# Kernel tuning notes

Measured on AMD Instinct MI355X. Metric: run time of the kernel, lower is better.

Reference implementation:

```python
import jax, jax.numpy as jnp
import numpy as np
import math

VOCAB, EMBED, RES = 50257, 512, 2048
B, T = 64, 512
LN_EPS = 1e-5


def setup_inputs() -> dict:
    key = jax.random.key(0)
    k_x, k_e, k_r, k_w = jax.random.split(key, 4)
    x = jax.random.randint(k_x, (B, T), 0, VOCAB)
    embed_weight = jax.random.normal(k_e, (VOCAB, EMBED), dtype=jnp.float32)
    R = jax.random.normal(k_r, (RES, RES), dtype=jnp.float32) / math.sqrt(RES) / 0.9
    Win = jax.random.normal(k_w, (EMBED, RES), dtype=jnp.float32) / math.sqrt(EMBED) / 0.9
    gamma = jnp.ones((RES,), dtype=jnp.float32)
    beta = jnp.zeros((RES,), dtype=jnp.float32)
    return {"x": x, "embed_weight": embed_weight, "R": R, "Win": Win,
            "gamma": gamma, "beta": beta}


def reference(x, embed_weight, R, Win, gamma, beta):
    emb = embed_weight[x]                              # [B, T, E]
    inp = jnp.einsum('bte,er->btr', emb, Win)          # [B, T, RES]

    def step(state, u_t):                              # state: [B, RES]
        new_state = jnp.tanh(state @ R + u_t)
        return new_state, None

    state0 = jnp.zeros((x.shape[0], R.shape[0]), dtype=emb.dtype)
    state, _ = jax.lax.scan(step, state0, jnp.swapaxes(inp, 0, 1))  # scan over T

    # LayerNorm over last dim (eps=1e-5, affine)
    mu = jnp.mean(state, axis=-1, keepdims=True)
    var = jnp.mean((state - mu) ** 2, axis=-1, keepdims=True)
    normed = (state - mu) / jnp.sqrt(var + LN_EPS)
    return normed * gamma + beta
```

## Files before the change

kernel.cpp:

```cpp
#include <hip/hip_runtime.h>

#define BB 64
#define TT 512
#define EE 512
#define RR 2048
#define CPW 32
#define RPG 16
#define NWGS 256
#define FPAD 16
#define SLOTB (BB * RR * 4)
#define GRPB  (RPG * RR * 4)
#define SPIN_CAP (1 << 20)

typedef _Float16 f16;
typedef f16 f16x8 __attribute__((ext_vector_type(8)));
typedef float f32x4 __attribute__((ext_vector_type(4)));

__device__ __forceinline__ void gload16(const void* g, void* l) {
  __builtin_amdgcn_global_load_lds(
      (const __attribute__((address_space(1))) void*)g,
      (__attribute__((address_space(3))) void*)l, 16, 0, 0);
}

__device__ __forceinline__ float fast_tanh(float v) {
  float e = __expf(2.0f * v);
  return 1.0f - 2.0f / (e + 1.0f);
}

__device__ __forceinline__ void storeS(f16* p, f16 h) {
  union { f16 h; unsigned short s; } u;
  u.h = h;
  __hip_atomic_store((unsigned short*)p, u.s, __ATOMIC_RELAXED, __HIP_MEMORY_SCOPE_AGENT);
}

__device__ __forceinline__ unsigned flag_ld(const unsigned* p) {
  return __hip_atomic_load(p, __ATOMIC_RELAXED, __HIP_MEMORY_SCOPE_AGENT);
}
__device__ __forceinline__ void flag_st(unsigned* p, unsigned v) {
  __hip_atomic_store(p, v, __ATOMIC_RELAXED, __HIP_MEMORY_SCOPE_AGENT);
}

__device__ __forceinline__ void issue8(f16x8* dst, unsigned voff, const f16* sbase) {
#pragma unroll
  for (int i = 0; i < 8; ++i)
    asm volatile("global_load_dwordx4 %0, %1, %2 offset:%c3"
                 : "=v"(dst[i]) : "v"(voff), "s"(sbase), "i"(64 * i) : "memory");
}

__device__ __forceinline__ float bypass_ldf(unsigned voff, const float* base) {
  float v;
  asm volatile("global_load_dword %0, %1, %2 sc0 sc1"
               : "=v"(v) : "v"(voff), "s"(base) : "memory");
  return v;
}

template <int N>
__device__ __forceinline__ void wait_vm() {
  asm volatile("s_waitcnt vmcnt(%c0)" :: "i"(N) : "memory");
  __builtin_amdgcn_sched_barrier(0);
}


__global__ void prep_emb(const int* __restrict__ x, const float* __restrict__ ew,
                         f16* __restrict__ emb) {
  const int row = blockIdx.x;
  const int tok = x[row];
  const float4* src = (const float4*)(ew + (size_t)tok * EE);
  f16* dst = emb + (size_t)row * EE;
  const int i = threadIdx.x;
  float4 v = src[i];
  union { f16 h[4]; unsigned long long u; } p;
  p.h[0] = (f16)v.x; p.h[1] = (f16)v.y; p.h[2] = (f16)v.z; p.h[3] = (f16)v.w;
  ((unsigned long long*)dst)[i] = p.u;
}

__global__ void prep_winT(const float* __restrict__ Win, f16* __restrict__ WinT) {
  const int i = blockIdx.x * blockDim.x + threadIdx.x;
  if (i < EE * RR) {
    const int k = i / RR, n = i % RR;
    WinT[(size_t)n * EE + k] = (f16)Win[i];
  }
}


__launch_bounds__(256, 1)
__global__ void proj_gemm(const f16* __restrict__ A, const f16* __restrict__ Bt,
                          float* __restrict__ U) {
  __shared__ f16 As[128 * 32];
  __shared__ f16 Bs[128 * 32];
  const int tid = threadIdx.x;
  const int wv = tid >> 6, l = tid & 63;
  const int m0 = blockIdx.x * 128, n0 = blockIdx.y * 128;
  const int wm = wv >> 1, wn = wv & 1;
  const int srow = tid >> 2, sc = tid & 3;
  const int r = l & 15, kb = l >> 4;
  f32x4 acc[4][4] = {};

  for (int k0 = 0; k0 < EE; k0 += 32) {
    __syncthreads();
#pragma unroll
    for (int q = 0; q < 2; ++q) {
      const int row = q * 64 + srow;
      const int cc = sc ^ (row & 3);
      gload16(A + (size_t)(m0 + row) * EE + k0 + cc * 8,
              (char*)As + q * 4096 + wv * 1024);
      gload16(Bt + (size_t)(n0 + row) * EE + k0 + cc * 8,
              (char*)Bs + q * 4096 + wv * 1024);
    }
    __syncthreads();
    f16x8 af[4], bf[4];
#pragma unroll
    for (int mi = 0; mi < 4; ++mi) {
      const int row = wm * 64 + mi * 16 + r;
      af[mi] = *(const f16x8*)&As[row * 32 + ((kb ^ (row & 3)) * 8)];
    }
#pragma unroll
    for (int ni = 0; ni < 4; ++ni) {
      const int row = wn * 64 + ni * 16 + r;
      bf[ni] = *(const f16x8*)&Bs[row * 32 + ((kb ^ (row & 3)) * 8)];
    }
#pragma unroll
    for (int mi = 0; mi < 4; ++mi)
#pragma unroll
      for (int ni = 0; ni < 4; ++ni)
        acc[mi][ni] = __builtin_amdgcn_mfma_f32_16x16x32_f16(af[mi], bf[ni], acc[mi][ni], 0, 0, 0);
  }
  const int rb = kb * 4;
#pragma unroll
  for (int mi = 0; mi < 4; ++mi)
#pragma unroll
    for (int ni = 0; ni < 4; ++ni)
#pragma unroll
      for (int j = 0; j < 4; ++j) {
        const int m = m0 + wm * 64 + mi * 16 + rb + j;
        const int n = n0 + wn * 64 + ni * 16 + r;
        const int b = m >> 9, t = m & 511;
        __builtin_nontemporal_store(acc[mi][ni][j], &U[(size_t)(t * BB + b) * RR + n]);
      }
}


__launch_bounds__(512, 1)
__global__ void scan_kernel(const float* __restrict__ R, float* Ub ,
                            f16* S1, unsigned* __restrict__ flg) {
  __shared__ __align__(16) char ldsbuf[CPW * RR * 2 + 16 * 1040];
  f16* Rt = (f16*)ldsbuf;
  const char* RtB = (const char*)ldsbuf;

  const int wg = blockIdx.x;
  const int xcd = wg & 7;
  const int grp = xcd >> 1;
  const int cw = ((wg >> 3) << 1) | (wg & 1);
  const int nbase = cw * CPW;
  const int rbase = grp * RPG;
  const int tid = threadIdx.x;
  const int wv = tid >> 6, l = tid & 63;
  unsigned* gflags = flg + (size_t)grp * 64 * FPAD;
  unsigned* myflag = gflags + cw * FPAD;
  const size_t grpoff = (size_t)grp * GRPB;

  __builtin_amdgcn_fence(__ATOMIC_ACQUIRE, "agent");

  const int mm = tid >> 5, cc = tid & 31;
  {
    const unsigned u0off = (unsigned)((((rbase + mm) * RR) + nbase + cc) * 4);
    float u0 = bypass_ldf(u0off, Ub);
    wait_vm<0>();
    storeS(&S1[(size_t)grp * (RPG * RR) + mm * RR + nbase + cc], (f16)fast_tanh(u0));
  }
  __syncthreads();
  if (tid == 0) flag_st(myflag, 1u);

  {
    const int c = tid & 31, kst = tid >> 5;
    for (int k = kst; k < RR; k += 16) {
      const float v = R[(size_t)k * RR + nbase + c];
      const int idx = ((k >> 5) << 10) + ((c >> 4) << 9) +
                      (((c & 15) << 2) + ((k >> 3) & 3)) * 8 + (k & 7);
      Rt[idx] = (f16)v;
    }
  }
  __syncthreads();

  const int r = l & 15, kb = l >> 4;
  const int kblk = (wv + cw) & 7;
  const unsigned voffA = (unsigned)(((r * RR) + (kblk << 8) + kb * 8) * 2);
  const int bb0 = (r * 4 + kb) * 16;
  const int ntr = cc >> 4;
  const int lred = (cc & 15) | ((mm >> 2) << 4);
  const int jred = mm & 3;
  const unsigned ubyte = (unsigned)((((rbase + mm) * RR) + nbase + cc) * 4);

  f16x8 abuf[8];

  for (int tau = 2; tau <= TT; ++tau) {
    const unsigned need = (unsigned)(tau - 1);

    {
      const unsigned* pp = &gflags[(size_t)(kblk * 8 + (l & 7)) * FPAD];
      unsigned fv = flag_ld(pp);
      int gd = 0;
      while (!__all(fv >= need) && ++gd < SPIN_CAP) {
        __builtin_amdgcn_s_sleep(1);
        fv = flag_ld(pp);
      }
    }

    const f16* sprev = (tau == 2)
        ? (const f16*)(S1 + (size_t)grp * (RPG * RR))
        : (const f16*)((const char*)Ub + (size_t)(tau - 3) * SLOTB + grpoff);
    f16* snext = (f16*)((char*)Ub + (size_t)(tau - 2) * SLOTB + grpoff);

    issue8(abuf, voffA, sprev);
    float uval;
    asm volatile("global_load_dword %0, %1, %2 sc0 sc1"
                 : "=v"(uval)
                 : "v"(ubyte), "s"((const float*)((const char*)Ub + (size_t)(tau - 1) * SLOTB))
                 : "memory");

    f32x4 acc0 = {0.f, 0.f, 0.f, 0.f}, acc1 = {0.f, 0.f, 0.f, 0.f};
#define KSTEP(ks)                                                              \
  {                                                                            \
    const int kc = (kblk << 3) + (ks);                                         \
    f16x8 b0 = *(const f16x8*)(RtB + kc * 2048 + bb0);                         \
    f16x8 b1 = *(const f16x8*)(RtB + kc * 2048 + 1024 + bb0);                  \
    acc0 = __builtin_amdgcn_mfma_f32_16x16x32_f16(abuf[ks], b0, acc0, 0, 0, 0);\
    acc1 = __builtin_amdgcn_mfma_f32_16x16x32_f16(abuf[ks], b1, acc1, 0, 0, 0);\
  }
    wait_vm<5>();
    KSTEP(0) KSTEP(1) KSTEP(2) KSTEP(3)
    wait_vm<1>();
    KSTEP(4) KSTEP(5) KSTEP(6) KSTEP(7)
#undef KSTEP
    wait_vm<0>();

    {
      char* red = ldsbuf + CPW * RR * 2;
      *(f32x4*)(red + (wv * 2 + 0) * 1040 + l * 16) = acc0;
      *(f32x4*)(red + (wv * 2 + 1) * 1040 + l * 16) = acc1;
    }
    __syncthreads();
    {
      const char* red = ldsbuf + CPW * RR * 2;
      float s = 0.f;
#pragma unroll
      for (int w = 0; w < 8; ++w)
        s += *(const float*)(red + (w * 2 + ntr) * 1040 + lred * 16 + jred * 4);
      storeS(&snext[(size_t)mm * RR + nbase + cc], (f16)fast_tanh(s + uval));
    }
    __syncthreads();
    if (tid == 0) flag_st(myflag, (unsigned)tau);
  }
}


__launch_bounds__(256, 1)
__global__ void ln_kernel(const char* __restrict__ slotbase, const float* __restrict__ gamma,
                          const float* __restrict__ beta, float* __restrict__ out) {
  const int b = blockIdx.x;
  const int tid = threadIdx.x;
  const f16* row = (const f16*)(slotbase + (size_t)(b >> 4) * GRPB) + (size_t)(b & 15) * RR;
  float vals[8];
  float lsum = 0.f, lsq = 0.f;
#pragma unroll
  for (int i = 0; i < 8; ++i) {
    float v = (float)row[tid + i * 256];
    vals[i] = v; lsum += v; lsq += v * v;
  }
#pragma unroll
  for (int off = 32; off >= 1; off >>= 1) {
    lsum += __shfl_xor(lsum, off);
    lsq  += __shfl_xor(lsq, off);
  }
  __shared__ float ps[4], pq[4];
  __shared__ float mu_s, rstd_s;
  const int wv = tid >> 6, l = tid & 63;
  if (l == 0) { ps[wv] = lsum; pq[wv] = lsq; }
  __syncthreads();
  if (tid == 0) {
    float s = 0.f, q = 0.f;
    for (int i = 0; i < 4; ++i) { s += ps[i]; q += pq[i]; }
    const float mu = s / RR;
    const float var = q / RR - mu * mu;
    mu_s = mu; rstd_s = rsqrtf(var + 1e-5f);
  }
  __syncthreads();
  const float mu = mu_s, rstd = rstd_s;
#pragma unroll
  for (int i = 0; i < 8; ++i) {
    const int idx = tid + i * 256;
    out[(size_t)b * RR + idx] = (vals[i] - mu) * rstd * gamma[idx] + beta[idx];
  }
}


extern "C" void kernel_launch(void* const* d_in, const int* in_sizes, int n_in,
                              void* d_out, int out_size, void* d_ws, size_t ws_size,
                              hipStream_t stream) {
  const int*   x     = (const int*)d_in[0];
  const float* ew    = (const float*)d_in[1];
  const float* Rm    = (const float*)d_in[2];
  const float* Win   = (const float*)d_in[3];
  const float* gamma = (const float*)d_in[4];
  const float* beta  = (const float*)d_in[5];

  const size_t U_OFF   = 0;
  const size_t EMB_OFF = 268435456;
  const size_t WT_OFF  = EMB_OFF + 33554432;
  const size_t S_OFF   = WT_OFF + 2097152;
  const size_t FLG_OFF = S_OFF + 524288;
  const size_t NEED    = FLG_OFF + 16384;
  if (ws_size < NEED) {
    hipMemsetAsync(d_out, 0, (size_t)out_size * 4, stream);
    return;
  }
  char* ws = (char*)d_ws;
  float*    Ubuf = (float*)(ws + U_OFF);
  f16*      emb  = (f16*)(ws + EMB_OFF);
  f16*      WinT = (f16*)(ws + WT_OFF);
  f16*      S1   = (f16*)(ws + S_OFF);
  unsigned* flg  = (unsigned*)(ws + FLG_OFF);

  hipMemsetAsync(flg, 0, 16384, stream);
  prep_emb<<<BB * TT, 128, 0, stream>>>(x, ew, emb);
  prep_winT<<<(EE * RR) / 256, 256, 0, stream>>>(Win, WinT);
  proj_gemm<<<dim3((BB * TT) / 128, RR / 128), 256, 0, stream>>>(emb, WinT, Ubuf);
  scan_kernel<<<NWGS, 512, 0, stream>>>(Rm, Ubuf, S1, flg);
  ln_kernel<<<BB, 256, 0, stream>>>(ws + (size_t)(TT - 2) * SLOTB,
                                    gamma, beta, (float*)d_out);
}
```

Baseline: 1.933 ms.

## Fuse input projection into recurrent scan kernel, drop standalone projection GEMM

Removes the separate projection GEMM that wrote a large fp32 U buffer. Two waves per scan workgroup now compute each step's input projection (emb x WinT) just in time with MFMA, from WinT fragments held in registers, and double-buffer the result in LDS. The state history is stored in its own f16 buffer. This removes a full-size GEMM launch and the fp32 U traffic, at the cost of extra per-step loads and MFMA work on the latency-critical scan path.

```diff
diff --git a/kernel.cpp b/kernel.cpp
--- a/kernel.cpp
+++ b/kernel.cpp
@@ -8,19 +8,13 @@
 #define RPG 16
 #define NWGS 256
 #define FPAD 16
-#define SLOTB (BB * RR * 4)
-#define GRPB  (RPG * RR * 4)
+#define SLOT2 (BB * RR * 2)
+#define GRP2  (RPG * RR * 2)
 #define SPIN_CAP (1 << 20)
 
 typedef _Float16 f16;
 typedef f16 f16x8 __attribute__((ext_vector_type(8)));
 typedef float f32x4 __attribute__((ext_vector_type(4)));
-
-__device__ __forceinline__ void gload16(const void* g, void* l) {
-  __builtin_amdgcn_global_load_lds(
-      (const __attribute__((address_space(1))) void*)g,
-      (__attribute__((address_space(3))) void*)l, 16, 0, 0);
-}
 
 __device__ __forceinline__ float fast_tanh(float v) {
   float e = __expf(2.0f * v);
@@ -46,12 +40,11 @@
     asm volatile("global_load_dwordx4 %0, %1, %2 offset:%c3"
                  : "=v"(dst[i]) : "v"(voff), "s"(sbase), "i"(64 * i) : "memory");
 }
-
-__device__ __forceinline__ float bypass_ldf(unsigned voff, const float* base) {
-  float v;
-  asm volatile("global_load_dword %0, %1, %2 sc0 sc1"
-               : "=v"(v) : "v"(voff), "s"(base) : "memory");
-  return v;
+__device__ __forceinline__ void issue16(f16x8* dst, unsigned voff, const f16* sbase) {
+#pragma unroll
+  for (int i = 0; i < 16; ++i)
+    asm volatile("global_load_dwordx4 %0, %1, %2 offset:%c3"
+                 : "=v"(dst[i]) : "v"(voff), "s"(sbase), "i"(64 * i) : "memory");
 }
 
 template <int N>
@@ -83,69 +76,14 @@
 }
 
 
-__launch_bounds__(256, 1)
-__global__ void proj_gemm(const f16* __restrict__ A, const f16* __restrict__ Bt,
-                          float* __restrict__ U) {
-  __shared__ f16 As[128 * 32];
-  __shared__ f16 Bs[128 * 32];
-  const int tid = threadIdx.x;
-  const int wv = tid >> 6, l = tid & 63;
-  const int m0 = blockIdx.x * 128, n0 = blockIdx.y * 128;
-  const int wm = wv >> 1, wn = wv & 1;
-  const int srow = tid >> 2, sc = tid & 3;
-  const int r = l & 15, kb = l >> 4;
-  f32x4 acc[4][4] = {};
-
-  for (int k0 = 0; k0 < EE; k0 += 32) {
-    __syncthreads();
-#pragma unroll
-    for (int q = 0; q < 2; ++q) {
-      const int row = q * 64 + srow;
-      const int cc = sc ^ (row & 3);
-      gload16(A + (size_t)(m0 + row) * EE + k0 + cc * 8,
-              (char*)As + q * 4096 + wv * 1024);
-      gload16(Bt + (size_t)(n0 + row) * EE + k0 + cc * 8,
-              (char*)Bs + q * 4096 + wv * 1024);
-    }
-    __syncthreads();
-    f16x8 af[4], bf[4];
-#pragma unroll
-    for (int mi = 0; mi < 4; ++mi) {
-      const int row = wm * 64 + mi * 16 + r;
-      af[mi] = *(const f16x8*)&As[row * 32 + ((kb ^ (row & 3)) * 8)];
-    }
-#pragma unroll
-    for (int ni = 0; ni < 4; ++ni) {
-      const int row = wn * 64 + ni * 16 + r;
-      bf[ni] = *(const f16x8*)&Bs[row * 32 + ((kb ^ (row & 3)) * 8)];
-    }
-#pragma unroll
-    for (int mi = 0; mi < 4; ++mi)
-#pragma unroll
-      for (int ni = 0; ni < 4; ++ni)
-        acc[mi][ni] = __builtin_amdgcn_mfma_f32_16x16x32_f16(af[mi], bf[ni], acc[mi][ni], 0, 0, 0);
-  }
-  const int rb = kb * 4;
-#pragma unroll
-  for (int mi = 0; mi < 4; ++mi)
-#pragma unroll
-    for (int ni = 0; ni < 4; ++ni)
-#pragma unroll
-      for (int j = 0; j < 4; ++j) {
-        const int m = m0 + wm * 64 + mi * 16 + rb + j;
-        const int n = n0 + wn * 64 + ni * 16 + r;
-        const int b = m >> 9, t = m & 511;
-        __builtin_nontemporal_store(acc[mi][ni][j], &U[(size_t)(t * BB + b) * RR + n]);
-      }
-}
-
-
 __launch_bounds__(512, 1)
-__global__ void scan_kernel(const float* __restrict__ R, float* Ub ,
-                            f16* S1, unsigned* __restrict__ flg) {
-  __shared__ __align__(16) char ldsbuf[CPW * RR * 2 + 16 * 1040];
+__global__ void scan_kernel(const float* __restrict__ R, f16* __restrict__ Sh,
+                            const f16* __restrict__ emb, const f16* __restrict__ WinT,
+                            unsigned* __restrict__ flg) {
+  __shared__ __align__(16) char ldsbuf[CPW * RR * 2 + 16 * 1040 + 2 * RPG * CPW * 4];
   f16* Rt = (f16*)ldsbuf;
   const char* RtB = (const char*)ldsbuf;
+  float* ubuf = (float*)(ldsbuf + CPW * RR * 2 + 16 * 1040);
 
   const int wg = blockIdx.x;
   const int xcd = wg & 7;
@@ -157,19 +95,12 @@
   const int wv = tid >> 6, l = tid & 63;
   unsigned* gflags = flg + (size_t)grp * 64 * FPAD;
   unsigned* myflag = gflags + cw * FPAD;
-  const size_t grpoff = (size_t)grp * GRPB;
+  f16* Sg = Sh + (size_t)grp * (RPG * RR);
 
   __builtin_amdgcn_fence(__ATOMIC_ACQUIRE, "agent");
 
+  const int r16 = l & 15, kb = l >> 4;
   const int mm = tid >> 5, cc = tid & 31;
-  {
-    const unsigned u0off = (unsigned)((((rbase + mm) * RR) + nbase + cc) * 4);
-    float u0 = bypass_ldf(u0off, Ub);
-    wait_vm<0>();
-    storeS(&S1[(size_t)grp * (RPG * RR) + mm * RR + nbase + cc], (f16)fast_tanh(u0));
-  }
-  __syncthreads();
-  if (tid == 0) flag_st(myflag, 1u);
 
   {
     const int c = tid & 31, kst = tid >> 5;
@@ -180,21 +111,55 @@
       Rt[idx] = (f16)v;
     }
   }
-  __syncthreads();
-
-  const int r = l & 15, kb = l >> 4;
+
+  f16x8 bfr[16];
+  if (wv < 2) {
+#pragma unroll
+    for (int kc = 0; kc < 16; ++kc)
+      bfr[kc] = *(const f16x8*)&WinT[(size_t)(nbase + wv * 16 + r16) * EE + kc * 32 + kb * 8];
+  }
+  __syncthreads();
+
+  if (wv < 2) {
+    f16x8 ebuf[16];
+#pragma unroll
+    for (int t01 = 0; t01 < 2; ++t01) {
+      const unsigned ve = (unsigned)(((((rbase + r16) * TT) + t01) * EE + kb * 8) * 2);
+      issue16(ebuf, ve, emb);
+      wait_vm<0>();
+      f32x4 au = {0.f, 0.f, 0.f, 0.f};
+#pragma unroll
+      for (int kc = 0; kc < 16; ++kc)
+        au = __builtin_amdgcn_mfma_f32_16x16x32_f16(ebuf[kc], bfr[kc], au, 0, 0, 0);
+#pragma unroll
+      for (int j = 0; j < 4; ++j)
+        ubuf[t01 * 512 + ((kb * 4 + j) * 32) + wv * 16 + r16] = au[j];
+    }
+  }
+  __syncthreads();
+
+  storeS(&Sg[(size_t)mm * RR + nbase + cc], (f16)fast_tanh(ubuf[mm * 32 + cc]));
+  __syncthreads();
+  if (tid == 0) flag_st(myflag, 1u);
+
   const int kblk = (wv + cw) & 7;
-  const unsigned voffA = (unsigned)(((r * RR) + (kblk << 8) + kb * 8) * 2);
-  const int bb0 = (r * 4 + kb) * 16;
+  const unsigned voffA = (unsigned)(((r16 * RR) + (kblk << 8) + kb * 8) * 2);
+  const int bb0 = (r16 * 4 + kb) * 16;
   const int ntr = cc >> 4;
   const int lred = (cc & 15) | ((mm >> 2) << 4);
   const int jred = mm & 3;
-  const unsigned ubyte = (unsigned)((((rbase + mm) * RR) + nbase + cc) * 4);
 
   f16x8 abuf[8];
 
   for (int tau = 2; tau <= TT; ++tau) {
     const unsigned need = (unsigned)(tau - 1);
+
+    f16x8 ebuf[16];
+    if (wv < 2) {
+      const int te = (tau < TT) ? tau : TT - 1;
+      const unsigned ve = (unsigned)(((((rbase + r16) * TT) + te) * EE + kb * 8) * 2);
+      issue16(ebuf, ve, emb);
+    }
 
     {
       const unsigned* pp = &gflags[(size_t)(kblk * 8 + (l & 7)) * FPAD];
@@ -206,17 +171,21 @@
       }
     }
 
-    const f16* sprev = (tau == 2)
-        ? (const f16*)(S1 + (size_t)grp * (RPG * RR))
-        : (const f16*)((const char*)Ub + (size_t)(tau - 3) * SLOTB + grpoff);
-    f16* snext = (f16*)((char*)Ub + (size_t)(tau - 2) * SLOTB + grpoff);
+    const f16* sprev = Sh + (size_t)(tau - 2) * (BB * RR) + (size_t)grp * (RPG * RR);
+    f16* snext = (f16*)((char*)Sh + (size_t)(tau - 1) * SLOT2) + (size_t)grp * (RPG * RR);
 
     issue8(abuf, voffA, sprev);
-    float uval;
-    asm volatile("global_load_dword %0, %1, %2 sc0 sc1"
-                 : "=v"(uval)
-                 : "v"(ubyte), "s"((const float*)((const char*)Ub + (size_t)(tau - 1) * SLOTB))
-                 : "memory");
+
+    if (wv < 2) {
+      wait_vm<8>();
+      f32x4 au = {0.f, 0.f, 0.f, 0.f};
+#pragma unroll
+      for (int kc = 0; kc < 16; ++kc)
+        au = __builtin_amdgcn_mfma_f32_16x16x32_f16(ebuf[kc], bfr[kc], au, 0, 0, 0);
+#pragma unroll
+      for (int j = 0; j < 4; ++j)
+        ubuf[(tau & 1) * 512 + ((kb * 4 + j) * 32) + wv * 16 + r16] = au[j];
+    }
 
     f32x4 acc0 = {0.f, 0.f, 0.f, 0.f}, acc1 = {0.f, 0.f, 0.f, 0.f};
 #define KSTEP(ks)                                                              \
@@ -227,12 +196,11 @@
     acc0 = __builtin_amdgcn_mfma_f32_16x16x32_f16(abuf[ks], b0, acc0, 0, 0, 0);\
     acc1 = __builtin_amdgcn_mfma_f32_16x16x32_f16(abuf[ks], b1, acc1, 0, 0, 0);\
   }
-    wait_vm<5>();
+    wait_vm<4>();
     KSTEP(0) KSTEP(1) KSTEP(2) KSTEP(3)
-    wait_vm<1>();
+    wait_vm<0>();
     KSTEP(4) KSTEP(5) KSTEP(6) KSTEP(7)
 #undef KSTEP
-    wait_vm<0>();
 
     {
       char* red = ldsbuf + CPW * RR * 2;
@@ -246,6 +214,7 @@
 #pragma unroll
       for (int w = 0; w < 8; ++w)
         s += *(const float*)(red + (w * 2 + ntr) * 1040 + lred * 16 + jred * 4);
+      const float uval = ubuf[((tau - 1) & 1) * 512 + mm * 32 + cc];
       storeS(&snext[(size_t)mm * RR + nbase + cc], (f16)fast_tanh(s + uval));
     }
     __syncthreads();
@@ -259,7 +228,7 @@
                           const float* __restrict__ beta, float* __restrict__ out) {
   const int b = blockIdx.x;
   const int tid = threadIdx.x;
-  const f16* row = (const f16*)(slotbase + (size_t)(b >> 4) * GRPB) + (size_t)(b & 15) * RR;
+  const f16* row = (const f16*)(slotbase + (size_t)(b >> 4) * GRP2) + (size_t)(b & 15) * RR;
   float vals[8];
   float lsum = 0.f, lsq = 0.f;
 #pragma unroll
@@ -304,28 +273,25 @@
   const float* gamma = (const float*)d_in[4];
   const float* beta  = (const float*)d_in[5];
 
-  const size_t U_OFF   = 0;
-  const size_t EMB_OFF = 268435456;
+  const size_t SH_OFF  = 0;
+  const size_t EMB_OFF = (size_t)TT * SLOT2;
   const size_t WT_OFF  = EMB_OFF + 33554432;
-  const size_t S_OFF   = WT_OFF + 2097152;
-  const size_t FLG_OFF = S_OFF + 524288;
+  const size_t FLG_OFF = WT_OFF + 2097152;
   const size_t NEED    = FLG_OFF + 16384;
   if (ws_size < NEED) {
     hipMemsetAsync(d_out, 0, (size_t)out_size * 4, stream);
     return;
   }
   char* ws = (char*)d_ws;
-  float*    Ubuf = (float*)(ws + U_OFF);
-  f16*      emb  = (f16*)(ws + EMB_OFF);
-  f16*      WinT = (f16*)(ws + WT_OFF);
-  f16*      S1   = (f16*)(ws + S_OFF);
-  unsigned* flg  = (unsigned*)(ws + FLG_OFF);
+  f16*      Shist = (f16*)(ws + SH_OFF);
+  f16*      emb   = (f16*)(ws + EMB_OFF);
+  f16*      WinT  = (f16*)(ws + WT_OFF);
+  unsigned* flg   = (unsigned*)(ws + FLG_OFF);
 
   hipMemsetAsync(flg, 0, 16384, stream);
   prep_emb<<<BB * TT, 128, 0, stream>>>(x, ew, emb);
   prep_winT<<<(EE * RR) / 256, 256, 0, stream>>>(Win, WinT);
-  proj_gemm<<<dim3((BB * TT) / 128, RR / 128), 256, 0, stream>>>(emb, WinT, Ubuf);
-  scan_kernel<<<NWGS, 512, 0, stream>>>(Rm, Ubuf, S1, flg);
-  ln_kernel<<<BB, 256, 0, stream>>>(ws + (size_t)(TT - 2) * SLOTB,
+  scan_kernel<<<NWGS, 512, 0, stream>>>(Rm, Shist, emb, WinT, flg);
+  ln_kernel<<<BB, 256, 0, stream>>>(ws + (size_t)(TT - 1) * SLOT2,
                                     gamma, beta, (float*)d_out);
 }
```

New measurement: 2.053 ms. 6.2% more time.
